# Kernel tuning notes

Hardware: AMD Instinct MI355X
Metric: run time of the kernel (lower is better)

## Reference

```python
import jax, jax.numpy as jnp
import numpy as np

N_NODES = 50000
N_EDGES = 4000   # hyperedges
NNZ = 400000
N_GRAPHS = 64
C = 1024
EPS = 1e-5


def _safe_inv(d):
    return jnp.where(d > 0, 1.0 / d, 0.0)


def hypergraph_conv(x, W, b, node_idx, hyperedge_idx):
    # PyG HypergraphConv (no attention, unit hyperedge weights):
    # out = D^{-1} H B^{-1} H^T (x W) + b
    h = x @ W                                              # [N, C]
    ones = jnp.ones(node_idx.shape[0], dtype=x.dtype)
    Dinv = _safe_inv(jax.ops.segment_sum(ones, node_idx, num_segments=N_NODES))
    Binv = _safe_inv(jax.ops.segment_sum(ones, hyperedge_idx, num_segments=N_EDGES))
    # node -> hyperedge
    m = jax.ops.segment_sum(h[node_idx], hyperedge_idx, num_segments=N_EDGES)
    m = m * Binv[:, None]                                  # [E, C]
    # hyperedge -> node
    out = jax.ops.segment_sum(m[hyperedge_idx], node_idx, num_segments=N_NODES)
    return out * Dinv[:, None] + b


def batch_norm(x, gamma, beta):
    mu = jnp.mean(x, axis=0)
    var = jnp.mean(jnp.square(x - mu), axis=0)
    return (x - mu) * jax.lax.rsqrt(var + EPS) * gamma + beta


def setup_inputs() -> dict:
    key = jax.random.key(0)
    ks = jax.random.split(key, 16)
    s = 1.0 / np.sqrt(C)
    inp = {
        "x": jax.random.normal(ks[0], (N_NODES, C), dtype=jnp.float32),
        "node_idx": jax.random.randint(ks[1], (NNZ,), 0, N_NODES, dtype=jnp.int32),
        "hyperedge_idx": jax.random.randint(ks[2], (NNZ,), 0, N_EDGES, dtype=jnp.int32),
        "batch": jnp.sort(jax.random.randint(ks[3], (N_NODES,), 0, N_GRAPHS, dtype=jnp.int32)),
        "W1": jax.random.normal(ks[4], (C, C), dtype=jnp.float32) * s,
        "b1": jnp.zeros((C,), dtype=jnp.float32),
        "W2": jax.random.normal(ks[5], (C, C), dtype=jnp.float32) * s,
        "b2": jnp.zeros((C,), dtype=jnp.float32),
        "W3": jax.random.normal(ks[6], (C, C), dtype=jnp.float32) * s,
        "b3": jnp.zeros((C,), dtype=jnp.float32),
        "g1": jnp.ones((C,), dtype=jnp.float32), "be1": jnp.zeros((C,), dtype=jnp.float32),
        "g2": jnp.ones((C,), dtype=jnp.float32), "be2": jnp.zeros((C,), dtype=jnp.float32),
        "g3": jnp.ones((C,), dtype=jnp.float32), "be3": jnp.zeros((C,), dtype=jnp.float32),
        "Wfc": jax.random.normal(ks[7], (C, 1), dtype=jnp.float32) * s,
        "bfc": jnp.zeros((1,), dtype=jnp.float32),
    }
    return inp


def reference(x, node_idx, hyperedge_idx, batch, W1, b1, W2, b2, W3, b3,
              g1, be1, g2, be2, g3, be3, Wfc, bfc):
    h = x
    for (W, b, g, be) in ((W1, b1, g1, be1), (W2, b2, g2, be2), (W3, b3, g3, be3)):
        h = hypergraph_conv(h, W, b, node_idx, hyperedge_idx)
        h = jax.nn.relu(batch_norm(h, g, be))  # dropout = identity (eval)
    # global_mean_pool over graph ids
    sums = jax.ops.segment_sum(h, batch, num_segments=N_GRAPHS)      # [G, C]
    cnt = jax.ops.segment_sum(jnp.ones((N_NODES,), h.dtype), batch, num_segments=N_GRAPHS)
    pooled = sums / jnp.maximum(cnt, 1.0)[:, None]
    out = (pooled @ Wfc + bfc).squeeze(-1)                            # [G]
    return jax.nn.sigmoid(out)
```

## Files before the change

### kernel.cpp

```cpp
#include <hip/hip_runtime.h>
#include <cstdint>
#include <cstddef>

#define N_NODES  50000
#define N_EDGES  4000
#define E_PAD    4096
#define NNZ_     400000
#define N_GRAPHS 64
#define C_DIM    1024
#define PB_BLOCKS 2048
#define BN_EPS   1e-5f

typedef float f32x4  __attribute__((ext_vector_type(4)));
typedef short bf16x4 __attribute__((ext_vector_type(4)));
typedef short bf16x8 __attribute__((ext_vector_type(8)));

__device__ __forceinline__ short f2bf(float f) {
  uint32_t u = __builtin_bit_cast(uint32_t, f);
  u += 0x7fffu + ((u >> 16) & 1u);
  return (short)(u >> 16);
}
__device__ __forceinline__ float bf2f(short s) {
  uint32_t u = ((uint32_t)(uint16_t)s) << 16;
  return __builtin_bit_cast(float, u);
}

__global__ void countDeg(const int* __restrict__ ni, const int* __restrict__ ei,
                         int* __restrict__ nd, int* __restrict__ ed) {
  int i = blockIdx.x * 256 + threadIdx.x;
  if (i < NNZ_) {
    atomicAdd(&nd[ni[i]], 1);
    atomicAdd(&ed[ei[i]], 1);
  }
}

__global__ void exscan(const int* __restrict__ deg, int* __restrict__ off, int n) {
  __shared__ int wsum[16];
  __shared__ int carry_s;
  int t = threadIdx.x, lane = t & 63, w = t >> 6;
  if (t == 0) carry_s = 0;
  __syncthreads();
  for (int base = 0; base < n; base += 1024) {
    int v = (base + t < n) ? deg[base + t] : 0;
    int x = v;
    #pragma unroll
    for (int d = 1; d < 64; d <<= 1) { int y = __shfl_up(x, d); if (lane >= d) x += y; }
    if (lane == 63) wsum[w] = x;
    __syncthreads();
    if (t < 16) {
      int y = wsum[t];
      #pragma unroll
      for (int d = 1; d < 16; d <<= 1) { int z = __shfl_up(y, d); if (t >= d) y += z; }
      wsum[t] = y;
    }
    __syncthreads();
    int c = carry_s;
    int incl = x + (w ? wsum[w - 1] : 0);
    if (base + t < n) off[base + t] = c + incl - v;
    int total = wsum[15];
    __syncthreads();
    if (t == 0) carry_s = c + total;
    __syncthreads();
  }
  if (threadIdx.x == 0) off[n] = carry_s;
}

__global__ void fillCSR(const int* __restrict__ ni, const int* __restrict__ ei,
                        const int* __restrict__ noff, const int* __restrict__ eoff,
                        int* __restrict__ ncur, int* __restrict__ ecur,
                        int* __restrict__ node_edge, int* __restrict__ edge_node) {
  int i = blockIdx.x * 256 + threadIdx.x;
  if (i < NNZ_) {
    int n = ni[i], e = ei[i];
    int pe = eoff[e] + atomicAdd(&ecur[e], 1);
    edge_node[pe] = n;
    int pn = noff[n] + atomicAdd(&ncur[n], 1);
    node_edge[pn] = e;
  }
}

__global__ void invdeg(const int* __restrict__ nd, const int* __restrict__ ed,
                       float* __restrict__ Dinv, float* __restrict__ Binv) {
  int i = blockIdx.x * 256 + threadIdx.x;
  if (i < N_NODES) { int d = nd[i]; Dinv[i] = d > 0 ? 1.f / (float)d : 0.f; }
  if (i < N_EDGES) { int d = ed[i]; Binv[i] = d > 0 ? 1.f / (float)d : 0.f; }
}

__global__ void convertWT(const float* __restrict__ Wm, short* __restrict__ WT) {
  __shared__ float tile[64][65];
  int tx = threadIdx.x & 63, ty = threadIdx.x >> 6;
  int kb = blockIdx.x * 64, nb = blockIdx.y * 64;
  #pragma unroll
  for (int j = 0; j < 64; j += 4)
    tile[j + ty][tx] = Wm[(size_t)(kb + j + ty) * C_DIM + nb + tx];
  __syncthreads();
  #pragma unroll
  for (int j = 0; j < 64; j += 4)
    WT[(size_t)(nb + j + ty) * C_DIM + kb + tx] = f2bf(tile[tx][j + ty]);
}

__global__ void convertX(const float* __restrict__ X, short* __restrict__ Hbf) {
  size_t idx = ((size_t)blockIdx.x * 256 + threadIdx.x) * 8;
  float v[8];
  *(f32x4*)&v[0] = *(const f32x4*)&X[idx];
  *(f32x4*)&v[4] = *(const f32x4*)&X[idx + 4];
  bf16x8 ov;
  #pragma unroll
  for (int j = 0; j < 8; ++j) ov[j] = f2bf(v[j]);
  *(bf16x8*)&Hbf[idx] = ov;
}

template <int BN>
__global__ __launch_bounds__(128) void phaseA_bn2(
    const short* __restrict__ Hbf, const int* __restrict__ eoff,
    const int* __restrict__ enode, const float* __restrict__ Binv,
    const float* __restrict__ sc, const float* __restrict__ sh,
    short* __restrict__ Mbf) {
  __shared__ int sidx[256];
  int t = threadIdx.x;
  int e = blockIdx.x;
  int c = t * 8;
  int beg = 0, len = 0;
  if (e < N_EDGES) {
    beg = eoff[e];
    len = eoff[e + 1] - beg;
  }
  float scl[8], shf[8];
  if (BN) {
    *(f32x4*)&scl[0] = *(const f32x4*)&sc[c];
    *(f32x4*)&scl[4] = *(const f32x4*)&sc[c + 4];
    *(f32x4*)&shf[0] = *(const f32x4*)&sh[c];
    *(f32x4*)&shf[4] = *(const f32x4*)&sh[c + 4];
  }
  float a0[8] = {0, 0, 0, 0, 0, 0, 0, 0};
  float a1[8] = {0, 0, 0, 0, 0, 0, 0, 0};
  for (int base = 0; base < len; base += 256) {
    int cnt = len - base;
    if (cnt > 256) cnt = 256;
    for (int j = t; j < cnt; j += 128) sidx[j] = enode[beg + base + j];
    __syncthreads();
    int i = 0;
    for (; i + 3 < cnt; i += 4) {
      int n0 = sidx[i], n1 = sidx[i + 1], n2 = sidx[i + 2], n3 = sidx[i + 3];
      bf16x8 v0 = *(const bf16x8*)&Hbf[(size_t)n0 * C_DIM + c];
      bf16x8 v1 = *(const bf16x8*)&Hbf[(size_t)n1 * C_DIM + c];
      bf16x8 v2 = *(const bf16x8*)&Hbf[(size_t)n2 * C_DIM + c];
      bf16x8 v3 = *(const bf16x8*)&Hbf[(size_t)n3 * C_DIM + c];
      #pragma unroll
      for (int j = 0; j < 8; ++j) {
        float f0 = bf2f(v0[j]), f1 = bf2f(v1[j]);
        float f2 = bf2f(v2[j]), f3 = bf2f(v3[j]);
        if (BN) {
          f0 = fmaxf(f0 * scl[j] + shf[j], 0.f);
          f1 = fmaxf(f1 * scl[j] + shf[j], 0.f);
          f2 = fmaxf(f2 * scl[j] + shf[j], 0.f);
          f3 = fmaxf(f3 * scl[j] + shf[j], 0.f);
        }
        a0[j] += f0 + f2;
        a1[j] += f1 + f3;
      }
    }
    for (; i < cnt; ++i) {
      bf16x8 v = *(const bf16x8*)&Hbf[(size_t)sidx[i] * C_DIM + c];
      #pragma unroll
      for (int j = 0; j < 8; ++j) {
        float f = bf2f(v[j]);
        if (BN) f = fmaxf(f * scl[j] + shf[j], 0.f);
        a0[j] += f;
      }
    }
    __syncthreads();
  }
  float bi = (e < N_EDGES) ? Binv[e] : 0.f;
  bf16x8 ov;
  #pragma unroll
  for (int j = 0; j < 8; ++j) ov[j] = f2bf((a0[j] + a1[j]) * bi);
  *(bf16x8*)&Mbf[(size_t)e * C_DIM + c] = ov;
}

__global__ __launch_bounds__(256) void gemm_bf16(const short* __restrict__ A,
                                                 const short* __restrict__ BT,
                                                 short* __restrict__ Cc) {
  __shared__ __align__(16) short As[2][128 * 32];
  __shared__ __align__(16) short Bs[2][128 * 32];
  const int tid = threadIdx.x;
  const int w = tid >> 6;
  const int lane = tid & 63;
  const int bm = blockIdx.x, bn = blockIdx.y;
  const int wr = w >> 1, wc = w & 1;
  const int fr = lane & 15, kg = lane >> 4;
  const int qa = w * 2;
  const int srow = lane >> 2;
  const int skof = (lane & 3) * 8;

  f32x4 acc[4][4] = {};

  auto stage = [&](int ks, int buf) {
    #pragma unroll
    for (int c2 = 0; c2 < 2; ++c2) {
      int q = qa + c2;
      int row = q * 16 + srow;
      size_t gA = (size_t)(bm * 128 + row) * C_DIM + ks * 32 + skof;
      size_t gB = (size_t)(bn * 128 + row) * C_DIM + ks * 32 + skof;
      __builtin_amdgcn_global_load_lds(
          (__attribute__((address_space(1))) void*)(A + gA),
          (__attribute__((address_space(3))) void*)(&As[buf][q * 512]), 16, 0, 0);
      __builtin_amdgcn_global_load_lds(
          (__attribute__((address_space(1))) void*)(BT + gB),
          (__attribute__((address_space(3))) void*)(&Bs[buf][q * 512]), 16, 0, 0);
    }
  };
  auto compute = [&](int buf) {
    bf16x8 a[4], b[4];
    #pragma unroll
    for (int m = 0; m < 4; ++m)
      a[m] = *(const bf16x8*)&As[buf][(wr * 64 + m * 16 + fr) * 32 + kg * 8];
    #pragma unroll
    for (int n = 0; n < 4; ++n)
      b[n] = *(const bf16x8*)&Bs[buf][(wc * 64 + n * 16 + fr) * 32 + kg * 8];
    #pragma unroll
    for (int m = 0; m < 4; ++m)
      #pragma unroll
      for (int n = 0; n < 4; ++n)
        acc[m][n] = __builtin_amdgcn_mfma_f32_16x16x32_bf16(a[m], b[n], acc[m][n], 0, 0, 0);
  };

  stage(0, 0);
  __syncthreads();
  for (int ks = 0; ks < 31; ++ks) {
    stage(ks + 1, (ks + 1) & 1);
    compute(ks & 1);
    __syncthreads();
  }
  compute(1);

  const int row0 = bm * 128 + wr * 64 + kg * 4;
  const int col0 = bn * 128 + wc * 64 + fr;
  #pragma unroll
  for (int m = 0; m < 4; ++m) {
    #pragma unroll
    for (int n = 0; n < 4; ++n) {
      int r = row0 + m * 16, cc = col0 + n * 16;
      #pragma unroll
      for (int j = 0; j < 4; ++j)
        Cc[(size_t)(r + j) * C_DIM + cc] = f2bf(acc[m][n][j]);
    }
  }
}

__global__ void phaseB_fused3(const short* __restrict__ M, const int* __restrict__ noff,
                              const int* __restrict__ nedge, const float* __restrict__ Dinv,
                              const float* __restrict__ bias, short* __restrict__ Hp,
                              float* __restrict__ ps, float* __restrict__ pq) {
  int t = threadIdx.x;
  int c = t * 4;
  int b = blockIdx.x;
  f32x4 bias4 = *(const f32x4*)&bias[c];
  f32x4 bsum = {0.f, 0.f, 0.f, 0.f}, bsq = {0.f, 0.f, 0.f, 0.f};
  for (int n = b; n < N_NODES; n += PB_BLOCKS) {
    int beg = noff[n], end = noff[n + 1];
    float a0[4] = {0, 0, 0, 0}, a1[4] = {0, 0, 0, 0};
    int i = beg;
    for (; i + 3 < end; i += 4) {
      int e0 = nedge[i], e1 = nedge[i + 1], e2 = nedge[i + 2], e3 = nedge[i + 3];
      bf16x4 v0 = *(const bf16x4*)&M[(size_t)e0 * C_DIM + c];
      bf16x4 v1 = *(const bf16x4*)&M[(size_t)e1 * C_DIM + c];
      bf16x4 v2 = *(const bf16x4*)&M[(size_t)e2 * C_DIM + c];
      bf16x4 v3 = *(const bf16x4*)&M[(size_t)e3 * C_DIM + c];
      #pragma unroll
      for (int j = 0; j < 4; ++j) {
        a0[j] += bf2f(v0[j]) + bf2f(v2[j]);
        a1[j] += bf2f(v1[j]) + bf2f(v3[j]);
      }
    }
    for (; i < end; ++i) {
      bf16x4 v = *(const bf16x4*)&M[(size_t)nedge[i] * C_DIM + c];
      #pragma unroll
      for (int j = 0; j < 4; ++j) a0[j] += bf2f(v[j]);
    }
    float di = Dinv[n];
    bf16x4 ob;
    f32x4 orr;
    #pragma unroll
    for (int j = 0; j < 4; ++j) {
      float o = (a0[j] + a1[j]) * di + bias4[j];
      ob[j] = f2bf(o);
      orr[j] = bf2f(ob[j]);
    }
    *(bf16x4*)&Hp[(size_t)n * C_DIM + c] = ob;
    bsum += orr;
    bsq += orr * orr;
  }
  *(f32x4*)&ps[(size_t)b * C_DIM + c] = bsum;
  *(f32x4*)&pq[(size_t)b * C_DIM + c] = bsq;
}

__global__ void reduceP(const float* __restrict__ ps, const float* __restrict__ pq,
                        float* __restrict__ ps2, float* __restrict__ pq2) {
  int i = blockIdx.x;
  int c = blockIdx.y * 256 + threadIdx.x;
  float s = 0.f, q = 0.f;
  for (int p = i * 256; p < (i + 1) * 256; ++p) {
    s += ps[(size_t)p * C_DIM + c];
    q += pq[(size_t)p * C_DIM + c];
  }
  ps2[(size_t)i * C_DIM + c] = s;
  pq2[(size_t)i * C_DIM + c] = q;
}

__global__ void bnfinal2(const float* __restrict__ ps2, const float* __restrict__ pq2,
                         const float* __restrict__ g, const float* __restrict__ be,
                         float* __restrict__ scale, float* __restrict__ shift) {
  int c = blockIdx.x * 256 + threadIdx.x;
  float s = 0.f, q = 0.f;
  #pragma unroll
  for (int p = 0; p < 8; ++p) {
    s += ps2[(size_t)p * C_DIM + c];
    q += pq2[(size_t)p * C_DIM + c];
  }
  const float invN = 1.f / (float)N_NODES;
  float mu = s * invN;
  float var = q * invN - mu * mu;
  float rs = rsqrtf(var + BN_EPS);
  float scl = g[c] * rs;
  scale[c] = scl;
  shift[c] = be[c] - mu * scl;
}

__global__ void finaldot_bf(const short* __restrict__ Hp, const float* __restrict__ sc,
                            const float* __restrict__ sh, const float* __restrict__ Wfc,
                            float* __restrict__ rows) {
  int row = blockIdx.x * 4 + (threadIdx.x >> 6);
  int lane = threadIdx.x & 63;
  if (row >= N_NODES) return;
  const short* hr = Hp + (size_t)row * C_DIM;
  float s = 0.f;
  #pragma unroll
  for (int j = 0; j < 2; ++j) {
    int c = j * 512 + lane * 8;
    bf16x8 v = *(const bf16x8*)&hr[c];
    float a[8], b[8], w[8];
    *(f32x4*)&a[0] = *(const f32x4*)&sc[c];
    *(f32x4*)&a[4] = *(const f32x4*)&sc[c + 4];
    *(f32x4*)&b[0] = *(const f32x4*)&sh[c];
    *(f32x4*)&b[4] = *(const f32x4*)&sh[c + 4];
    *(f32x4*)&w[0] = *(const f32x4*)&Wfc[c];
    *(f32x4*)&w[4] = *(const f32x4*)&Wfc[c + 4];
    #pragma unroll
    for (int k = 0; k < 8; ++k)
      s += fmaxf(bf2f(v[k]) * a[k] + b[k], 0.f) * w[k];
  }
  #pragma unroll
  for (int off = 32; off; off >>= 1) s += __shfl_down(s, off);
  if (lane == 0) rows[row] = s;
}

__global__ void poolbin(const float* __restrict__ rows, const int* __restrict__ batch,
                        float* __restrict__ gsum, int* __restrict__ gcnt) {
  __shared__ float bins[N_GRAPHS];
  __shared__ int cbin[N_GRAPHS];
  int t = threadIdx.x;
  if (t < N_GRAPHS) { bins[t] = 0.f; cbin[t] = 0; }
  __syncthreads();
  int quad = blockIdx.x * 256 + t;
  if (quad * 4 < N_NODES) {
    f32x4 r = *(const f32x4*)&rows[quad * 4];
    int4 bi = *(const int4*)&batch[quad * 4];
    int g0 = bi.x;
    float acc = r[0];
    int cc = 1;
    int gn[3] = {bi.y, bi.z, bi.w};
    float rn[3] = {r[1], r[2], r[3]};
    #pragma unroll
    for (int j = 0; j < 3; ++j) {
      if (gn[j] == g0) { acc += rn[j]; ++cc; }
      else {
        atomicAdd(&bins[g0], acc);
        atomicAdd(&cbin[g0], cc);
        g0 = gn[j]; acc = rn[j]; cc = 1;
      }
    }
    atomicAdd(&bins[g0], acc);
    atomicAdd(&cbin[g0], cc);
  }
  __syncthreads();
  if (t < N_GRAPHS && cbin[t] > 0) {
    atomicAdd(&gsum[t], bins[t]);
    atomicAdd(&gcnt[t], cbin[t]);
  }
}

__global__ void finalout(const float* __restrict__ gsum, const int* __restrict__ gcnt,
                         const float* __restrict__ bfc, float* __restrict__ out) {
  int g = threadIdx.x;
  float cnt = (float)(gcnt[g] > 0 ? gcnt[g] : 1);
  float v = gsum[g] / cnt + bfc[0];
  out[g] = 1.f / (1.f + expf(-v));
}

extern "C" void kernel_launch(void* const* d_in, const int* in_sizes, int n_in,
                              void* d_out, int out_size, void* d_ws, size_t ws_size,
                              hipStream_t stream) {
  const float* x        = (const float*)d_in[0];
  const int*   node_idx = (const int*)d_in[1];
  const int*   hedge_idx= (const int*)d_in[2];
  const int*   batch    = (const int*)d_in[3];
  const float* W[3]  = {(const float*)d_in[4], (const float*)d_in[6], (const float*)d_in[8]};
  const float* bb[3] = {(const float*)d_in[5], (const float*)d_in[7], (const float*)d_in[9]};
  const float* g[3]  = {(const float*)d_in[10], (const float*)d_in[12], (const float*)d_in[14]};
  const float* be[3] = {(const float*)d_in[11], (const float*)d_in[13], (const float*)d_in[15]};
  const float* Wfc   = (const float*)d_in[16];
  const float* bfc   = (const float*)d_in[17];
  float* out = (float*)d_out;

  char* ws = (char*)d_ws;
  size_t o = 0;
  auto take = [&](size_t bytes) -> char* {
    char* p = ws + o;
    o += (bytes + 255) & ~(size_t)255;
    return p;
  };
  short* Xbf  = (short*)take((size_t)N_NODES * C_DIM * 2);
  short* Hp   = (short*)take((size_t)N_NODES * C_DIM * 2);
  short* Mbf  = (short*)take((size_t)E_PAD * C_DIM * 2);
  short* WT   = (short*)take((size_t)C_DIM * C_DIM * 2);
  short* Mw   = (short*)take((size_t)E_PAD * C_DIM * 2);
  char*  zgrp = take(432512);
  int*   node_deg = (int*)zgrp;
  int*   edge_deg = (int*)(zgrp + 200000);
  int*   node_cur = (int*)(zgrp + 216000);
  int*   edge_cur = (int*)(zgrp + 416000);
  float* gsum     = (float*)(zgrp + 432000);
  int*   gcnt     = (int*)(zgrp + 432256);
  int* node_off  = (int*)take((N_NODES + 1) * 4);
  int* edge_off  = (int*)take((N_EDGES + 1) * 4);
  int* node_edge = (int*)take((size_t)NNZ_ * 4);
  int* edge_node = (int*)take((size_t)NNZ_ * 4);
  float* Dinv = (float*)take(N_NODES * 4);
  float* Binv = (float*)take(N_EDGES * 4);
  float* scale = (float*)take(4096);
  float* shift = (float*)take(4096);
  float* part_s = (float*)take((size_t)PB_BLOCKS * C_DIM * 4);
  float* part_q = (float*)take((size_t)PB_BLOCKS * C_DIM * 4);
  float* ps2    = (float*)take((size_t)8 * C_DIM * 4);
  float* pq2    = (float*)take((size_t)8 * C_DIM * 4);
  float* rows   = (float*)take((size_t)N_NODES * 4);

  hipMemsetAsync(zgrp, 0, 432512, stream);

  countDeg<<<(NNZ_ + 255) / 256, 256, 0, stream>>>(node_idx, hedge_idx, node_deg, edge_deg);
  exscan<<<1, 1024, 0, stream>>>(edge_deg, edge_off, N_EDGES);
  exscan<<<1, 1024, 0, stream>>>(node_deg, node_off, N_NODES);
  fillCSR<<<(NNZ_ + 255) / 256, 256, 0, stream>>>(node_idx, hedge_idx, node_off, edge_off,
                                                  node_cur, edge_cur, node_edge, edge_node);
  invdeg<<<(N_NODES + 255) / 256, 256, 0, stream>>>(node_deg, edge_deg, Dinv, Binv);

  const int cgrid = (int)((size_t)N_NODES * C_DIM / (8 * 256));
  convertX<<<cgrid, 256, 0, stream>>>(x, Xbf);
  for (int L = 0; L < 3; ++L) {
    if (L == 0)
      phaseA_bn2<0><<<E_PAD, 128, 0, stream>>>(Xbf, edge_off, edge_node, Binv,
                                               nullptr, nullptr, Mbf);
    else
      phaseA_bn2<1><<<E_PAD, 128, 0, stream>>>(Hp, edge_off, edge_node, Binv,
                                               scale, shift, Mbf);
    convertWT<<<dim3(16, 16), 256, 0, stream>>>(W[L], WT);
    gemm_bf16<<<dim3(E_PAD / 128, C_DIM / 128), 256, 0, stream>>>(Mbf, WT, Mw);
    phaseB_fused3<<<PB_BLOCKS, 256, 0, stream>>>(Mw, node_off, node_edge, Dinv, bb[L],
                                                 Hp, part_s, part_q);
    reduceP<<<dim3(8, 4), 256, 0, stream>>>(part_s, part_q, ps2, pq2);
    bnfinal2<<<4, 256, 0, stream>>>(ps2, pq2, g[L], be[L], scale, shift);
  }
  finaldot_bf<<<(N_NODES + 3) / 4, 256, 0, stream>>>(Hp, scale, shift, Wfc, rows);
  poolbin<<<(N_NODES / 4 + 255) / 256, 256, 0, stream>>>(rows, batch, gsum, gcnt);
  finalout<<<1, 64, 0, stream>>>(gsum, gcnt, bfc, out);
}
```

Before: 1.116 ms.

## Split node feature storage into channel halves and run phaseA per half

Result: no change. 1.114 ms (-0.2%).

```diff
diff --git a/kernel.cpp b/kernel.cpp
--- a/kernel.cpp
+++ b/kernel.cpp
@@ -8,6 +8,7 @@
 #define NNZ_     400000
 #define N_GRAPHS 64
 #define C_DIM    1024
+#define HALF_C   512
 #define PB_BLOCKS 2048
 #define BN_EPS   1e-5f
 
@@ -101,81 +102,79 @@
 
 __global__ void convertX(const float* __restrict__ X, short* __restrict__ Hbf) {
   size_t idx = ((size_t)blockIdx.x * 256 + threadIdx.x) * 8;
+  int node = (int)(idx >> 10);
+  int c = (int)(idx & 1023);
+  int half = c >> 9, off = c & 511;
   float v[8];
   *(f32x4*)&v[0] = *(const f32x4*)&X[idx];
   *(f32x4*)&v[4] = *(const f32x4*)&X[idx + 4];
   bf16x8 ov;
   #pragma unroll
   for (int j = 0; j < 8; ++j) ov[j] = f2bf(v[j]);
-  *(bf16x8*)&Hbf[idx] = ov;
+  *(bf16x8*)&Hbf[((size_t)half * N_NODES + node) * HALF_C + off] = ov;
 }
 
 template <int BN>
-__global__ __launch_bounds__(128) void phaseA_bn2(
+__global__ __launch_bounds__(64) void phaseA_bn3(
     const short* __restrict__ Hbf, const int* __restrict__ eoff,
     const int* __restrict__ enode, const float* __restrict__ Binv,
     const float* __restrict__ sc, const float* __restrict__ sh,
-    short* __restrict__ Mbf) {
-  __shared__ int sidx[256];
+    short* __restrict__ Mbf, int half) {
   int t = threadIdx.x;
   int e = blockIdx.x;
-  int c = t * 8;
-  int beg = 0, len = 0;
-  if (e < N_EDGES) {
-    beg = eoff[e];
-    len = eoff[e + 1] - beg;
-  }
+  int off = t * 8;
+  int gc = half * HALF_C + off;
+  if (e >= N_EDGES) {
+    bf16x8 z = {0, 0, 0, 0, 0, 0, 0, 0};
+    *(bf16x8*)&Mbf[(size_t)e * C_DIM + gc] = z;
+    return;
+  }
+  const short* __restrict__ src = Hbf + (size_t)half * N_NODES * HALF_C;
   float scl[8], shf[8];
   if (BN) {
-    *(f32x4*)&scl[0] = *(const f32x4*)&sc[c];
-    *(f32x4*)&scl[4] = *(const f32x4*)&sc[c + 4];
-    *(f32x4*)&shf[0] = *(const f32x4*)&sh[c];
-    *(f32x4*)&shf[4] = *(const f32x4*)&sh[c + 4];
-  }
+    *(f32x4*)&scl[0] = *(const f32x4*)&sc[gc];
+    *(f32x4*)&scl[4] = *(const f32x4*)&sc[gc + 4];
+    *(f32x4*)&shf[0] = *(const f32x4*)&sh[gc];
+    *(f32x4*)&shf[4] = *(const f32x4*)&sh[gc + 4];
+  }
+  int beg = eoff[e], end = eoff[e + 1];
   float a0[8] = {0, 0, 0, 0, 0, 0, 0, 0};
   float a1[8] = {0, 0, 0, 0, 0, 0, 0, 0};
-  for (int base = 0; base < len; base += 256) {
-    int cnt = len - base;
-    if (cnt > 256) cnt = 256;
-    for (int j = t; j < cnt; j += 128) sidx[j] = enode[beg + base + j];
-    __syncthreads();
-    int i = 0;
-    for (; i + 3 < cnt; i += 4) {
-      int n0 = sidx[i], n1 = sidx[i + 1], n2 = sidx[i + 2], n3 = sidx[i + 3];
-      bf16x8 v0 = *(const bf16x8*)&Hbf[(size_t)n0 * C_DIM + c];
-      bf16x8 v1 = *(const bf16x8*)&Hbf[(size_t)n1 * C_DIM + c];
-      bf16x8 v2 = *(const bf16x8*)&Hbf[(size_t)n2 * C_DIM + c];
-      bf16x8 v3 = *(const bf16x8*)&Hbf[(size_t)n3 * C_DIM + c];
-      #pragma unroll
-      for (int j = 0; j < 8; ++j) {
-        float f0 = bf2f(v0[j]), f1 = bf2f(v1[j]);
-        float f2 = bf2f(v2[j]), f3 = bf2f(v3[j]);
-        if (BN) {
-          f0 = fmaxf(f0 * scl[j] + shf[j], 0.f);
-          f1 = fmaxf(f1 * scl[j] + shf[j], 0.f);
-          f2 = fmaxf(f2 * scl[j] + shf[j], 0.f);
-          f3 = fmaxf(f3 * scl[j] + shf[j], 0.f);
-        }
-        a0[j] += f0 + f2;
-        a1[j] += f1 + f3;
+  int i = beg;
+  for (; i + 3 < end; i += 4) {
+    int n0 = enode[i], n1 = enode[i + 1], n2 = enode[i + 2], n3 = enode[i + 3];
+    bf16x8 v0 = *(const bf16x8*)&src[(size_t)n0 * HALF_C + off];
+    bf16x8 v1 = *(const bf16x8*)&src[(size_t)n1 * HALF_C + off];
+    bf16x8 v2 = *(const bf16x8*)&src[(size_t)n2 * HALF_C + off];
+    bf16x8 v3 = *(const bf16x8*)&src[(size_t)n3 * HALF_C + off];
+    #pragma unroll
+    for (int j = 0; j < 8; ++j) {
+      float f0 = bf2f(v0[j]), f1 = bf2f(v1[j]);
+      float f2 = bf2f(v2[j]), f3 = bf2f(v3[j]);
+      if (BN) {
+        f0 = fmaxf(f0 * scl[j] + shf[j], 0.f);
+        f1 = fmaxf(f1 * scl[j] + shf[j], 0.f);
+        f2 = fmaxf(f2 * scl[j] + shf[j], 0.f);
+        f3 = fmaxf(f3 * scl[j] + shf[j], 0.f);
       }
-    }
-    for (; i < cnt; ++i) {
-      bf16x8 v = *(const bf16x8*)&Hbf[(size_t)sidx[i] * C_DIM + c];
-      #pragma unroll
-      for (int j = 0; j < 8; ++j) {
-        float f = bf2f(v[j]);
-        if (BN) f = fmaxf(f * scl[j] + shf[j], 0.f);
-        a0[j] += f;
-      }
-    }
-    __syncthreads();
-  }
-  float bi = (e < N_EDGES) ? Binv[e] : 0.f;
+      a0[j] += f0 + f2;
+      a1[j] += f1 + f3;
+    }
+  }
+  for (; i < end; ++i) {
+    bf16x8 v = *(const bf16x8*)&src[(size_t)enode[i] * HALF_C + off];
+    #pragma unroll
+    for (int j = 0; j < 8; ++j) {
+      float f = bf2f(v[j]);
+      if (BN) f = fmaxf(f * scl[j] + shf[j], 0.f);
+      a0[j] += f;
+    }
+  }
+  float bi = Binv[e];
   bf16x8 ov;
   #pragma unroll
   for (int j = 0; j < 8; ++j) ov[j] = f2bf((a0[j] + a1[j]) * bi);
-  *(bf16x8*)&Mbf[(size_t)e * C_DIM + c] = ov;
+  *(bf16x8*)&Mbf[(size_t)e * C_DIM + gc] = ov;
 }
 
 __global__ __launch_bounds__(256) void gemm_bf16(const short* __restrict__ A,
@@ -254,6 +253,8 @@
                               float* __restrict__ ps, float* __restrict__ pq) {
   int t = threadIdx.x;
   int c = t * 4;
+  int half = c >> 9, off = c & 511;
+  short* __restrict__ Hdst = Hp + (size_t)half * N_NODES * HALF_C;
   int b = blockIdx.x;
   f32x4 bias4 = *(const f32x4*)&bias[c];
   f32x4 bsum = {0.f, 0.f, 0.f, 0.f}, bsq = {0.f, 0.f, 0.f, 0.f};
@@ -287,7 +288,7 @@
       ob[j] = f2bf(o);
       orr[j] = bf2f(ob[j]);
     }
-    *(bf16x4*)&Hp[(size_t)n * C_DIM + c] = ob;
+    *(bf16x4*)&Hdst[(size_t)n * HALF_C + off] = ob;
     bsum += orr;
     bsq += orr * orr;
   }
@@ -333,12 +334,11 @@
   int row = blockIdx.x * 4 + (threadIdx.x >> 6);
   int lane = threadIdx.x & 63;
   if (row >= N_NODES) return;
-  const short* hr = Hp + (size_t)row * C_DIM;
   float s = 0.f;
   #pragma unroll
   for (int j = 0; j < 2; ++j) {
-    int c = j * 512 + lane * 8;
-    bf16x8 v = *(const bf16x8*)&hr[c];
+    int c = j * HALF_C + lane * 8;
+    bf16x8 v = *(const bf16x8*)&Hp[((size_t)j * N_NODES + row) * HALF_C + lane * 8];
     float a[8], b[8], w[8];
     *(f32x4*)&a[0] = *(const f32x4*)&sc[c];
     *(f32x4*)&a[4] = *(const f32x4*)&sc[c + 4];
@@ -458,12 +458,15 @@
   const int cgrid = (int)((size_t)N_NODES * C_DIM / (8 * 256));
   convertX<<<cgrid, 256, 0, stream>>>(x, Xbf);
   for (int L = 0; L < 3; ++L) {
-    if (L == 0)
-      phaseA_bn2<0><<<E_PAD, 128, 0, stream>>>(Xbf, edge_off, edge_node, Binv,
-                                               nullptr, nullptr, Mbf);
-    else
-      phaseA_bn2<1><<<E_PAD, 128, 0, stream>>>(Hp, edge_off, edge_node, Binv,
-                                               scale, shift, Mbf);
+    const short* src = (L == 0) ? Xbf : Hp;
+    for (int half = 0; half < 2; ++half) {
+      if (L == 0)
+        phaseA_bn3<0><<<E_PAD, 64, 0, stream>>>(src, edge_off, edge_node, Binv,
+                                                nullptr, nullptr, Mbf, half);
+      else
+        phaseA_bn3<1><<<E_PAD, 64, 0, stream>>>(src, edge_off, edge_node, Binv,
+                                                scale, shift, Mbf, half);
+    }
     convertWT<<<dim3(16, 16), 256, 0, stream>>>(W[L], WT);
     gemm_bf16<<<dim3(E_PAD / 128, C_DIM / 128), 256, 0, stream>>>(Mbf, WT, Mw);
     phaseB_fused3<<<PB_BLOCKS, 256, 0, stream>>>(Mw, node_off, node_edge, Dinv, bb[L],
```
